# Optimization experiments

Hardware: AMD Instinct MI355X
Metric: run time of the kernel (lower is better)

Reference implementation:

```python
import jax, jax.numpy as jnp
import numpy as np

DIM = 1024
NUM_HEADS = 16
BATCH = 4
SEQ = 2048
SCALE = (DIM // NUM_HEADS) ** -0.5
MASK_VAL = -10000000.0


def setup_inputs() -> dict:
    key = jax.random.key(0)
    k1, k2, k3, k4 = jax.random.split(key, 4)
    inputs = jax.random.normal(k1, (BATCH, SEQ, DIM), dtype=jnp.float32)
    # xavier-ish scaling for weights
    W_qkv = jax.random.normal(k2, (3 * DIM, DIM), dtype=jnp.float32) * (1.0 / np.sqrt(DIM))
    W_fc = jax.random.normal(k3, (DIM, DIM), dtype=jnp.float32) * (1.0 / np.sqrt(DIM))
    b_fc = jnp.zeros((DIM,), dtype=jnp.float32)
    padding_mask = jax.random.randint(k4, (BATCH, SEQ), 0, 2, dtype=jnp.int32)
    return {"inputs": inputs, "W_qkv": W_qkv, "W_fc": W_fc, "b_fc": b_fc,
            "padding_mask": padding_mask}


def reference(inputs, W_qkv, W_fc, b_fc, padding_mask):
    B, N, C = inputs.shape
    H = NUM_HEADS
    Dh = C // H
    # qkv projection (torch Linear: x @ W.T), [B,N,3C]
    qkv = jnp.einsum('bnc,oc->bno', inputs, W_qkv)
    qkv = qkv.reshape(B, N, 3, H, Dh).transpose(2, 0, 3, 1, 4)  # [3,B,H,N,Dh]
    q, k, v = qkv[0], qkv[1], qkv[2]
    att = jnp.einsum('bhqd,bhkd->bhqk', q, k) * SCALE  # [B,H,N,N]
    mask = padding_mask[:, None, None, :]              # [B,1,1,N]
    att = jnp.where(mask > 0, jnp.float32(MASK_VAL), att)
    att = jax.nn.softmax(att, axis=-1)
    x = jnp.einsum('bhqk,bhkd->bhqd', att, v)          # [B,H,N,Dh]
    x = x.transpose(0, 2, 1, 3).reshape(B, N, C)       # [B,N,C]
    out = jnp.einsum('bnc,oc->bno', x, W_fc) + b_fc
    return out
```

## Files before the change

kernel.cpp:

```cpp
#include <hip/hip_runtime.h>
#include <stdint.h>

constexpr int kDim  = 1024;
constexpr int kH    = 16;
constexpr int kB    = 4;
constexpr int kSeq  = 2048;
constexpr int kDh   = 64;
constexpr int kMTot = kB * kSeq;
constexpr int kNQkv = 3 * kDim;
constexpr float kScale = 0.125f;
constexpr float kLog2e = 1.44269504088896f;
constexpr float kC1    = kScale * kLog2e;
constexpr float kMaxSub = 10.0f;
constexpr float kMk2Un   = -kMaxSub * kLog2e;
constexpr float kMk2Mask = -1.0e9f;
constexpr int kPld = 72;
constexpr int kCld = 136;

typedef __attribute__((ext_vector_type(8))) short short8;
typedef __attribute__((ext_vector_type(4))) float floatx4;

__device__ __forceinline__ unsigned short f2bf(float f) {
  union { float f; unsigned u; } v; v.f = f;
  unsigned r = v.u + 0x7fffu + ((v.u >> 16) & 1u);
  return (unsigned short)(r >> 16);
}
__device__ __forceinline__ unsigned short f2bf_fast(float f) {
  union { float f; unsigned u; } v; v.f = f;
  return (unsigned short)((v.u + 0x8000u) >> 16);
}
__device__ __forceinline__ float vexp2(float x) {
  float r; asm("v_exp_f32 %0, %1" : "=v"(r) : "v"(x)); return r;
}
__device__ __forceinline__ void gl2lds16(const void* g, void* l) {
  __builtin_amdgcn_global_load_lds(
      (const __attribute__((address_space(1))) unsigned int*)g,
      (__attribute__((address_space(3))) unsigned int*)l, 16, 0, 0);
}

__global__ void __launch_bounds__(256) cvt_scan(
    const float4* __restrict__ x, const float4* __restrict__ wq,
    const float4* __restrict__ wf,
    ushort4* __restrict__ xb, ushort4* __restrict__ wqb, ushort4* __restrict__ wfb,
    const int* __restrict__ pm, int* __restrict__ cidx, int* __restrict__ nkd) {
  const int X4  = (kMTot * kDim) / 4;
  const int WQ4 = (kNQkv * kDim) / 4;
  const int NCVT = 12288;
  if (blockIdx.x >= NCVT) {
    const int b = blockIdx.x - NCVT;
    const int t = threadIdx.x;
    const int lane = t & 63, wv = t >> 6;
    __shared__ int wsum[4];
    __shared__ int woff[5];
    int base = t * 8;
    int keep[8]; int cnt = 0;
#pragma unroll
    for (int j = 0; j < 8; j++) {
      keep[j] = (pm[b * kSeq + base + j] <= 0) ? 1 : 0;
      cnt += keep[j];
    }
    int pre = cnt;
#pragma unroll
    for (int off = 1; off < 64; off <<= 1) {
      int v = __shfl_up(pre, off, 64);
      if (lane >= off) pre += v;
    }
    int excl = pre - cnt;
    if (lane == 63) wsum[wv] = pre;
    __syncthreads();
    if (t == 0) {
      int s = 0;
#pragma unroll
      for (int w = 0; w < 4; w++) { woff[w] = s; s += wsum[w]; }
      woff[4] = s;
      nkd[b] = s;
    }
    __syncthreads();
    const int nk = woff[4];
    int kp = woff[wv] + excl;
#pragma unroll
    for (int j = 0; j < 8; j++) {
      int n = base + j;
      int pos = keep[j] ? kp : nk + (n - kp);
      cidx[b * kSeq + pos] = b * kSeq + n;
      kp += keep[j];
    }
    return;
  }
  int i = blockIdx.x * 256 + threadIdx.x;
  float4 v; ushort4* dst;
  if (i < X4)            { v = x[i];             dst = xb  + i; }
  else if (i < X4 + WQ4) { v = wq[i - X4];       dst = wqb + (i - X4); }
  else                   { v = wf[i - X4 - WQ4]; dst = wfb + (i - X4 - WQ4); }
  ushort4 o;
  o.x = f2bf(v.x); o.y = f2bf(v.y); o.z = f2bf(v.z); o.w = f2bf(v.w);
  *dst = o;
}

__device__ __forceinline__ void gemm128_mainloop(
    const unsigned short* const arow[4], const unsigned short* __restrict__ Bw,
    int tN, unsigned short* As, unsigned short* Bs, floatx4 acc[4][4]) {
  const int t = threadIdx.x;
  const int lane = t & 63, wv = t >> 6;
  const int wm = (wv >> 1) << 6, wn = (wv & 1) << 6;
  const int lrow = lane & 15, quad = lane >> 4, l7 = lane & 7;
  const int srow = t >> 3;
  const int pu8 = (t & 7) * 8;
  const int lu8 = ((t & 7) ^ (srow & 7)) * 8;
  const int off0 = (quad ^ l7) * 8;

  floatx4 zero = {0.f, 0.f, 0.f, 0.f};
#pragma unroll
  for (int mi = 0; mi < 4; mi++)
#pragma unroll
    for (int ni = 0; ni < 4; ni++) acc[mi][ni] = zero;

  for (int k0 = 0; k0 < kDim; k0 += 64) {
#pragma unroll
    for (int p = 0; p < 4; ++p) {
      int r = srow + p * 32;
      gl2lds16(arow[p] + k0 + lu8, As + r * 64 + pu8);
      gl2lds16(Bw + (int64_t)(tN + r) * kDim + k0 + lu8, Bs + r * 64 + pu8);
    }
    __syncthreads();
#pragma unroll
    for (int kk = 0; kk < 64; kk += 32) {
      short8 af[4], bf[4];
#pragma unroll
      for (int mi = 0; mi < 4; mi++)
        af[mi] = *(const short8*)(As + (wm + mi * 16 + lrow) * 64 + (off0 ^ kk));
#pragma unroll
      for (int ni = 0; ni < 4; ni++)
        bf[ni] = *(const short8*)(Bs + (wn + ni * 16 + lrow) * 64 + (off0 ^ kk));
#pragma unroll
      for (int mi = 0; mi < 4; mi++)
#pragma unroll
        for (int ni = 0; ni < 4; ni++)
          acc[mi][ni] = __builtin_amdgcn_mfma_f32_16x16x32_bf16(af[mi], bf[ni], acc[mi][ni], 0, 0, 0);
    }
    __syncthreads();
  }
}

__global__ void __launch_bounds__(256) gemm_qkv(
    const unsigned short* __restrict__ xb, const unsigned short* __restrict__ wqb,
    const int* __restrict__ cidx, const int* __restrict__ nkd,
    unsigned short* __restrict__ qb, unsigned short* __restrict__ kb,
    unsigned short* __restrict__ vtb) {
  const int tN = blockIdx.x * 128, tM = blockIdx.y * 128;
  const int which = tN >> 10;
  if (which != 0) {
    int b = tM >> 11, local = tM & 2047;
    if (local >= nkd[b]) return;
  }
  extern __shared__ __attribute__((aligned(16))) unsigned short smem[];
  unsigned short* As = smem;
  unsigned short* Bs = smem + 128 * 64;
  floatx4 acc[4][4];

  const int t = threadIdx.x, srow = t >> 3;
  const unsigned short* arow[4];
#pragma unroll
  for (int p = 0; p < 4; p++) {
    int r = tM + srow + p * 32;
    int rid = (which == 0) ? r : cidx[r];
    arow[p] = xb + (int64_t)rid * kDim;
  }
  gemm128_mainloop(arow, wqb, tN, As, Bs, acc);

  const int lane = t & 63, wv = t >> 6;
  const int wm = (wv >> 1) << 6, wn = (wv & 1) << 6;
  const int lrow = lane & 15, quad = lane >> 4;
  unsigned short* Cs = smem;
  const bool vblk = (which == 2);
#pragma unroll
  for (int ni = 0; ni < 4; ni++) {
    int c = wn + ni * 16 + lrow;
#pragma unroll
    for (int mi = 0; mi < 4; mi++) {
#pragma unroll
      for (int r = 0; r < 4; r++) {
        int row = wm + mi * 16 + quad * 4 + r;
        unsigned short val = f2bf(acc[mi][ni][r]);
        if (!vblk) Cs[row * kCld + c] = val;
        else       Cs[c * kCld + row] = val;
      }
    }
  }
  __syncthreads();
  const int mj8 = lane >> 3;
  const int chunk = lane & 7;
#pragma unroll
  for (int half = 0; half < 2; half++) {
#pragma unroll
    for (int g = 0; g < 4; g++) {
      int mjr = wv * 32 + g * 8 + mj8;
      short8 vec = *(const short8*)(Cs + mjr * kCld + half * 64 + chunk * 8);
      if (!vblk) {
        int i = tM + mjr;
        int bb = i >> 11, n = i & 2047;
        int o = tN + half * 64 + chunk * 8;
        int h = (o >> 6) & 15;
        int64_t base = (int64_t)((bb << 4) + h) << 17;
        unsigned short* dst = (which == 0 ? qb : kb) + base + (int64_t)n * 64 + (o & 63);
        *(short8*)dst = vec;
      } else {
        int o = tN + mjr;
        int h = (o >> 6) & 15, d = o & 63;
        int bb = tM >> 11;
        int n0 = (tM & 2047) + half * 64 + chunk * 8;
        unsigned short* dst = vtb + (((int64_t)((bb << 4) + h)) << 17)
                              + (int64_t)d * 2048 + n0;
        *(short8*)dst = vec;
      }
    }
  }
}

__global__ void __launch_bounds__(256, 4) attn(
    const unsigned short* __restrict__ qb, const unsigned short* __restrict__ kb,
    const unsigned short* __restrict__ vtb, const int* __restrict__ nkd,
    unsigned short* __restrict__ xab) {
  __shared__ __attribute__((aligned(16))) unsigned short Ks[64 * 64];
  __shared__ __attribute__((aligned(16))) unsigned short Vs[64 * 64];
  __shared__ __attribute__((aligned(16))) unsigned short Ps[4][2][16 * kPld];

  const int t = threadIdx.x, lane = t & 63, wv = t >> 6;
  const int lrow = lane & 15, quad = lane >> 4, l7 = lane & 7;
  const int qblk = blockIdx.x & 15, bh = blockIdx.x >> 4;
  const int b = bh >> 4, h = bh & 15;
  const int q0 = qblk * 128;
  const int srow = t >> 3;
  const int pu8 = (t & 7) * 8;
  const int lu8 = ((t & 7) ^ (srow & 7)) * 8;
  const int off0 = (quad ^ l7) * 8;

  const int nk  = nkd[b];
  const int nkt = (nk + 63) >> 6;

  const unsigned short* Qb0 = qb + ((int64_t)bh * kSeq + q0 + wv * 16 + lrow) * kDh;
  short8 qf[2][2];
  qf[0][0] = *(const short8*)(Qb0 + quad * 8);
  qf[0][1] = *(const short8*)(Qb0 + 32 + quad * 8);
  qf[1][0] = *(const short8*)(Qb0 + 64 * kDh + quad * 8);
  qf[1][1] = *(const short8*)(Qb0 + 64 * kDh + 32 + quad * 8);

  float l_run[2][4];
  floatx4 o_acc[2][4];
  floatx4 zero = {0.f, 0.f, 0.f, 0.f};
#pragma unroll
  for (int t2 = 0; t2 < 2; t2++) {
#pragma unroll
    for (int r = 0; r < 4; r++) l_run[t2][r] = 0.f;
#pragma unroll
    for (int di = 0; di < 4; di++) o_acc[t2][di] = zero;
  }

  const unsigned short* Kbase = kb  + (int64_t)bh * kSeq * kDh;
  const unsigned short* Vbase = vtb + (int64_t)bh * kDh * kSeq;

  for (int kt = 0; kt < nkt; ++kt) {
    const int k0 = kt * 64;
    {
      int r0 = srow, r1 = srow + 32;
      gl2lds16(Kbase + (int64_t)(k0 + r0) * kDh + lu8, Ks + r0 * 64 + pu8);
      gl2lds16(Kbase + (int64_t)(k0 + r1) * kDh + lu8, Ks + r1 * 64 + pu8);
      gl2lds16(Vbase + (int64_t)r0 * kSeq + k0 + lu8,  Vs + r0 * 64 + pu8);
      gl2lds16(Vbase + (int64_t)r1 * kSeq + k0 + lu8,  Vs + r1 * 64 + pu8);
    }
    __syncthreads();

    floatx4 s[2][4];
#pragma unroll
    for (int ni = 0; ni < 4; ni++) {
      const unsigned short* Kr = Ks + (ni * 16 + lrow) * 64;
      short8 kf0 = *(const short8*)(Kr + off0);
      short8 kf1 = *(const short8*)(Kr + (off0 ^ 32));
#pragma unroll
      for (int t2 = 0; t2 < 2; t2++) {
        floatx4 tmp = __builtin_amdgcn_mfma_f32_16x16x32_bf16(qf[t2][0], kf0, zero, 0, 0, 0);
        s[t2][ni]   = __builtin_amdgcn_mfma_f32_16x16x32_bf16(qf[t2][1], kf1, tmp, 0, 0, 0);
      }
    }
    float mk2[4];
#pragma unroll
    for (int c = 0; c < 4; c++)
      mk2[c] = (k0 + c * 16 + lrow < nk) ? kMk2Un : kMk2Mask;

#pragma unroll
    for (int t2 = 0; t2 < 2; t2++) {
      unsigned short* Pw = &Ps[wv][t2][0];
#pragma unroll
      for (int r = 0; r < 4; r++) {
        int prow = (quad * 4 + r) * kPld + lrow;
#pragma unroll
        for (int c = 0; c < 4; c++) {
          float p = vexp2(fmaf(s[t2][c][r], kC1, mk2[c]));
          l_run[t2][r] += p;
          Pw[prow + c * 16] = f2bf_fast(p);
        }
      }
    }
    asm volatile("s_waitcnt lgkmcnt(0)" ::: "memory");

#pragma unroll
    for (int ks = 0; ks < 2; ks++) {
      short8 pf0 = *(const short8*)(&Ps[wv][0][0] + lrow * kPld + ks * 32 + quad * 8);
      short8 pf1 = *(const short8*)(&Ps[wv][1][0] + lrow * kPld + ks * 32 + quad * 8);
      const int voff = off0 ^ (ks * 32);
#pragma unroll
      for (int di = 0; di < 4; di++) {
        short8 vf = *(const short8*)(Vs + (di * 16 + lrow) * 64 + voff);
        o_acc[0][di] = __builtin_amdgcn_mfma_f32_16x16x32_bf16(pf0, vf, o_acc[0][di], 0, 0, 0);
        o_acc[1][di] = __builtin_amdgcn_mfma_f32_16x16x32_bf16(pf1, vf, o_acc[1][di], 0, 0, 0);
      }
    }
    __syncthreads();
  }

#pragma unroll
  for (int t2 = 0; t2 < 2; t2++) {
#pragma unroll
    for (int r = 0; r < 4; r++) {
      float l = l_run[t2][r];
      l += __shfl_xor(l, 1, 64);
      l += __shfl_xor(l, 2, 64);
      l += __shfl_xor(l, 4, 64);
      l += __shfl_xor(l, 8, 64);
      float inv = 1.0f / l;
      int n = q0 + t2 * 64 + wv * 16 + quad * 4 + r;
      int64_t rowbase = ((int64_t)b * kSeq + n) * kDim + h * kDh;
#pragma unroll
      for (int di = 0; di < 4; di++)
        xab[rowbase + di * 16 + lrow] = f2bf(o_acc[t2][di][r] * inv);
    }
  }
}

__global__ void __launch_bounds__(256) gemm_fc(
    const unsigned short* __restrict__ xab, const unsigned short* __restrict__ wfb,
    const float* __restrict__ bfc, float* __restrict__ out) {
  __shared__ __attribute__((aligned(16))) unsigned short As[128 * 64];
  __shared__ __attribute__((aligned(16))) unsigned short Bs[64 * 64];
  const int tN = blockIdx.x * 64, tM = blockIdx.y * 128;
  const int t = threadIdx.x;
  const int lane = t & 63, wv = t >> 6;
  const int wm = (wv >> 1) << 6, wn = (wv & 1) << 5;
  const int lrow = lane & 15, quad = lane >> 4, l7 = lane & 7;
  const int srow = t >> 3;
  const int pu8 = (t & 7) * 8;
  const int lu8 = ((t & 7) ^ (srow & 7)) * 8;
  const int off0 = (quad ^ l7) * 8;

  floatx4 acc[4][2];
  floatx4 zero = {0.f, 0.f, 0.f, 0.f};
#pragma unroll
  for (int mi = 0; mi < 4; mi++)
#pragma unroll
    for (int ni = 0; ni < 2; ni++) acc[mi][ni] = zero;

  for (int k0 = 0; k0 < kDim; k0 += 64) {
#pragma unroll
    for (int p = 0; p < 4; ++p) {
      int r = srow + p * 32;
      gl2lds16(xab + (int64_t)(tM + r) * kDim + k0 + lu8, As + r * 64 + pu8);
    }
#pragma unroll
    for (int p = 0; p < 2; ++p) {
      int r = srow + p * 32;
      gl2lds16(wfb + (int64_t)(tN + r) * kDim + k0 + lu8, Bs + r * 64 + pu8);
    }
    __syncthreads();
#pragma unroll
    for (int kk = 0; kk < 64; kk += 32) {
      short8 af[4], bf[2];
#pragma unroll
      for (int mi = 0; mi < 4; mi++)
        af[mi] = *(const short8*)(As + (wm + mi * 16 + lrow) * 64 + (off0 ^ kk));
#pragma unroll
      for (int ni = 0; ni < 2; ni++)
        bf[ni] = *(const short8*)(Bs + (wn + ni * 16 + lrow) * 64 + (off0 ^ kk));
#pragma unroll
      for (int mi = 0; mi < 4; mi++)
#pragma unroll
        for (int ni = 0; ni < 2; ni++)
          acc[mi][ni] = __builtin_amdgcn_mfma_f32_16x16x32_bf16(af[mi], bf[ni], acc[mi][ni], 0, 0, 0);
    }
    __syncthreads();
  }

#pragma unroll
  for (int ni = 0; ni < 2; ni++) {
    int o = tN + wn + ni * 16 + lrow;
    float bias = bfc[o];
#pragma unroll
    for (int mi = 0; mi < 4; mi++) {
#pragma unroll
      for (int r = 0; r < 4; r++) {
        int i = tM + wm + mi * 16 + quad * 4 + r;
        out[(int64_t)i * kDim + o] = acc[mi][ni][r] + bias;
      }
    }
  }
}

extern "C" void kernel_launch(void* const* d_in, const int* in_sizes, int n_in,
                              void* d_out, int out_size, void* d_ws, size_t ws_size,
                              hipStream_t stream) {
  (void)in_sizes; (void)n_in; (void)out_size; (void)ws_size;
  const float* x    = (const float*)d_in[0];
  const float* wqkv = (const float*)d_in[1];
  const float* wfc  = (const float*)d_in[2];
  const float* bfc  = (const float*)d_in[3];
  const int*   pm   = (const int*)d_in[4];
  float* out = (float*)d_out;

  char* ws = (char*)d_ws;
  unsigned short* xb  = (unsigned short*)(ws);
  unsigned short* wqb = (unsigned short*)(ws + 16777216);
  unsigned short* wfb = (unsigned short*)(ws + 23068672);
  unsigned short* qb  = (unsigned short*)(ws + 25165824);
  unsigned short* kb  = (unsigned short*)(ws + 41943040);
  unsigned short* vtb = (unsigned short*)(ws + 58720256);
  int*            cidx= (int*)(ws + 75497472);
  int*            nkd = (int*)(ws + 75530240);
  unsigned short* xab = xb;

  cvt_scan<<<12288 + kB, 256, 0, stream>>>(
      (const float4*)x, (const float4*)wqkv, (const float4*)wfc,
      (ushort4*)xb, (ushort4*)wqb, (ushort4*)wfb, pm, cidx, nkd);
  gemm_qkv<<<dim3(kNQkv / 128, kMTot / 128), 256, 128 * kCld * 2, stream>>>(
      xb, wqb, cidx, nkd, qb, kb, vtb);
  attn<<<kB * kH * (kSeq / 128), 256, 0, stream>>>(qb, kb, vtb, nkd, xab);
  gemm_fc<<<dim3(kDim / 64, kMTot / 128), 256, 0, stream>>>(xab, wfb, bfc, out);
}
```

Before: 241.3 us.

## Load K/V fragments directly from global in attention; stage FC output through LDS

The attention kernel drops its shared-memory K/V tiles and the two block barriers per key tile, and each wave reads its MFMA K and V fragments straight from global memory (relying on L1/L2 reuse across waves). The score/softmax loop is restructured per 16-key chunk, the block index ordering is swapped so blocks sharing a query block but differing in head are adjacent, and the occupancy hint is removed. The FC GEMM epilogue now stages results in dynamic LDS and writes coalesced float4 rows instead of scattered scalar stores. This trades shared-memory staging for more global/cache traffic and redundant loads across waves.

```diff
diff --git a/kernel.cpp b/kernel.cpp
--- a/kernel.cpp
+++ b/kernel.cpp
@@ -16,6 +16,7 @@
 constexpr float kMk2Mask = -1.0e9f;
 constexpr int kPld = 72;
 constexpr int kCld = 136;
+constexpr int kCldF = 68;
 
 typedef __attribute__((ext_vector_type(8))) short short8;
 typedef __attribute__((ext_vector_type(4))) float floatx4;
@@ -217,23 +218,17 @@
   }
 }
 
-__global__ void __launch_bounds__(256, 4) attn(
+__global__ void __launch_bounds__(256) attn(
     const unsigned short* __restrict__ qb, const unsigned short* __restrict__ kb,
     const unsigned short* __restrict__ vtb, const int* __restrict__ nkd,
     unsigned short* __restrict__ xab) {
-  __shared__ __attribute__((aligned(16))) unsigned short Ks[64 * 64];
-  __shared__ __attribute__((aligned(16))) unsigned short Vs[64 * 64];
   __shared__ __attribute__((aligned(16))) unsigned short Ps[4][2][16 * kPld];
 
   const int t = threadIdx.x, lane = t & 63, wv = t >> 6;
-  const int lrow = lane & 15, quad = lane >> 4, l7 = lane & 7;
-  const int qblk = blockIdx.x & 15, bh = blockIdx.x >> 4;
+  const int lrow = lane & 15, quad = lane >> 4;
+  const int bh = blockIdx.x & 63, qblk = blockIdx.x >> 6;
   const int b = bh >> 4, h = bh & 15;
   const int q0 = qblk * 128;
-  const int srow = t >> 3;
-  const int pu8 = (t & 7) * 8;
-  const int lu8 = ((t & 7) ^ (srow & 7)) * 8;
-  const int off0 = (quad ^ l7) * 8;
 
   const int nk  = nkd[b];
   const int nkt = (nk + 63) >> 6;
@@ -256,66 +251,47 @@
     for (int di = 0; di < 4; di++) o_acc[t2][di] = zero;
   }
 
-  const unsigned short* Kbase = kb  + (int64_t)bh * kSeq * kDh;
-  const unsigned short* Vbase = vtb + (int64_t)bh * kDh * kSeq;
+  const unsigned short* Kf0 = kb  + (int64_t)bh * kSeq * kDh + lrow * kDh + quad * 8;
+  const unsigned short* Vf0 = vtb + (int64_t)bh * kDh * kSeq + lrow * kSeq + quad * 8;
+  unsigned short* Pw0 = &Ps[wv][0][0];
+  unsigned short* Pw1 = &Ps[wv][1][0];
 
   for (int kt = 0; kt < nkt; ++kt) {
     const int k0 = kt * 64;
-    {
-      int r0 = srow, r1 = srow + 32;
-      gl2lds16(Kbase + (int64_t)(k0 + r0) * kDh + lu8, Ks + r0 * 64 + pu8);
-      gl2lds16(Kbase + (int64_t)(k0 + r1) * kDh + lu8, Ks + r1 * 64 + pu8);
-      gl2lds16(Vbase + (int64_t)r0 * kSeq + k0 + lu8,  Vs + r0 * 64 + pu8);
-      gl2lds16(Vbase + (int64_t)r1 * kSeq + k0 + lu8,  Vs + r1 * 64 + pu8);
-    }
-    __syncthreads();
-
-    floatx4 s[2][4];
 #pragma unroll
     for (int ni = 0; ni < 4; ni++) {
-      const unsigned short* Kr = Ks + (ni * 16 + lrow) * 64;
-      short8 kf0 = *(const short8*)(Kr + off0);
-      short8 kf1 = *(const short8*)(Kr + (off0 ^ 32));
-#pragma unroll
-      for (int t2 = 0; t2 < 2; t2++) {
-        floatx4 tmp = __builtin_amdgcn_mfma_f32_16x16x32_bf16(qf[t2][0], kf0, zero, 0, 0, 0);
-        s[t2][ni]   = __builtin_amdgcn_mfma_f32_16x16x32_bf16(qf[t2][1], kf1, tmp, 0, 0, 0);
-      }
-    }
-    float mk2[4];
-#pragma unroll
-    for (int c = 0; c < 4; c++)
-      mk2[c] = (k0 + c * 16 + lrow < nk) ? kMk2Un : kMk2Mask;
-
-#pragma unroll
-    for (int t2 = 0; t2 < 2; t2++) {
-      unsigned short* Pw = &Ps[wv][t2][0];
+      const unsigned short* Kr = Kf0 + (int64_t)(k0 + ni * 16) * kDh;
+      short8 kf0 = *(const short8*)(Kr);
+      short8 kf1 = *(const short8*)(Kr + 32);
+      floatx4 s0 = __builtin_amdgcn_mfma_f32_16x16x32_bf16(qf[0][0], kf0, zero, 0, 0, 0);
+      s0 = __builtin_amdgcn_mfma_f32_16x16x32_bf16(qf[0][1], kf1, s0, 0, 0, 0);
+      floatx4 s1 = __builtin_amdgcn_mfma_f32_16x16x32_bf16(qf[1][0], kf0, zero, 0, 0, 0);
+      s1 = __builtin_amdgcn_mfma_f32_16x16x32_bf16(qf[1][1], kf1, s1, 0, 0, 0);
+      float mk2 = (k0 + ni * 16 + lrow < nk) ? kMk2Un : kMk2Mask;
+      int pcol = ni * 16 + lrow;
 #pragma unroll
       for (int r = 0; r < 4; r++) {
-        int prow = (quad * 4 + r) * kPld + lrow;
-#pragma unroll
-        for (int c = 0; c < 4; c++) {
-          float p = vexp2(fmaf(s[t2][c][r], kC1, mk2[c]));
-          l_run[t2][r] += p;
-          Pw[prow + c * 16] = f2bf_fast(p);
-        }
+        float p0 = vexp2(fmaf(s0[r], kC1, mk2));
+        float p1 = vexp2(fmaf(s1[r], kC1, mk2));
+        l_run[0][r] += p0; l_run[1][r] += p1;
+        int prow = (quad * 4 + r) * kPld + pcol;
+        Pw0[prow] = f2bf_fast(p0);
+        Pw1[prow] = f2bf_fast(p1);
       }
     }
     asm volatile("s_waitcnt lgkmcnt(0)" ::: "memory");
 
 #pragma unroll
     for (int ks = 0; ks < 2; ks++) {
-      short8 pf0 = *(const short8*)(&Ps[wv][0][0] + lrow * kPld + ks * 32 + quad * 8);
-      short8 pf1 = *(const short8*)(&Ps[wv][1][0] + lrow * kPld + ks * 32 + quad * 8);
-      const int voff = off0 ^ (ks * 32);
+      short8 pf0 = *(const short8*)(Pw0 + lrow * kPld + ks * 32 + quad * 8);
+      short8 pf1 = *(const short8*)(Pw1 + lrow * kPld + ks * 32 + quad * 8);
 #pragma unroll
       for (int di = 0; di < 4; di++) {
-        short8 vf = *(const short8*)(Vs + (di * 16 + lrow) * 64 + voff);
+        short8 vf = *(const short8*)(Vf0 + (int64_t)(di * 16) * kSeq + k0 + ks * 32);
         o_acc[0][di] = __builtin_amdgcn_mfma_f32_16x16x32_bf16(pf0, vf, o_acc[0][di], 0, 0, 0);
         o_acc[1][di] = __builtin_amdgcn_mfma_f32_16x16x32_bf16(pf1, vf, o_acc[1][di], 0, 0, 0);
       }
     }
-    __syncthreads();
   }
 
 #pragma unroll
@@ -340,8 +316,10 @@
 __global__ void __launch_bounds__(256) gemm_fc(
     const unsigned short* __restrict__ xab, const unsigned short* __restrict__ wfb,
     const float* __restrict__ bfc, float* __restrict__ out) {
-  __shared__ __attribute__((aligned(16))) unsigned short As[128 * 64];
-  __shared__ __attribute__((aligned(16))) unsigned short Bs[64 * 64];
+  extern __shared__ __attribute__((aligned(16))) unsigned short smem[];
+  unsigned short* As = smem;
+  unsigned short* Bs = smem + 128 * 64;
+  float* Csf = (float*)smem;
   const int tN = blockIdx.x * 64, tM = blockIdx.y * 128;
   const int t = threadIdx.x;
   const int lane = t & 63, wv = t >> 6;
@@ -389,16 +367,36 @@
     __syncthreads();
   }
 
-#pragma unroll
-  for (int ni = 0; ni < 2; ni++) {
-    int o = tN + wn + ni * 16 + lrow;
-    float bias = bfc[o];
-#pragma unroll
-    for (int mi = 0; mi < 4; mi++) {
-#pragma unroll
-      for (int r = 0; r < 4; r++) {
-        int i = tM + wm + mi * 16 + quad * 4 + r;
-        out[(int64_t)i * kDim + o] = acc[mi][ni][r] + bias;
+  const int mj8 = lane >> 3, chunk = lane & 7;
+  float bias[2];
+#pragma unroll
+  for (int ni = 0; ni < 2; ni++) bias[ni] = bfc[tN + wn + ni * 16 + lrow];
+#pragma unroll
+  for (int pass = 0; pass < 2; pass++) {
+    if (pass) __syncthreads();
+    if ((wv >> 1) == pass) {
+#pragma unroll
+      for (int ni = 0; ni < 2; ni++) {
+        int c = wn + ni * 16 + lrow;
+#pragma unroll
+        for (int mi = 0; mi < 4; mi++) {
+#pragma unroll
+          for (int r = 0; r < 4; r++) {
+            int l = mi * 16 + quad * 4 + r;
+            Csf[l * kCldF + c] = acc[mi][ni][r] + bias[ni];
+          }
+        }
+      }
+    }
+    __syncthreads();
+#pragma unroll
+    for (int g = 0; g < 2; g++) {
+      int l = wv * 16 + g * 8 + mj8;
+      int i = tM + pass * 64 + l;
+#pragma unroll
+      for (int half = 0; half < 2; half++) {
+        float4 v = *(const float4*)(Csf + l * kCldF + half * 32 + chunk * 4);
+        *(float4*)(out + (int64_t)i * kDim + tN + half * 32 + chunk * 4) = v;
       }
     }
   }
@@ -432,5 +430,5 @@
   gemm_qkv<<<dim3(kNQkv / 128, kMTot / 128), 256, 128 * kCld * 2, stream>>>(
       xb, wqb, cidx, nkd, qb, kb, vtb);
   attn<<<kB * kH * (kSeq / 128), 256, 0, stream>>>(qb, kb, vtb, nkd, xab);
-  gemm_fc<<<dim3(kDim / 64, kMTot / 128), 256, 0, stream>>>(xab, wfb, bfc, out);
-}
+  gemm_fc<<<dim3(kDim / 64, kMTot / 128), 256, 24576, stream>>>(xab, wfb, bfc, out);
+}
```

Result: slower. 320.0 us (+32.6%).
